# Kernel tuning notes

Hardware: AMD Instinct MI355X
Metric: run time of the kernel (lower is better)

Reference implementation:

```python
import jax, jax.numpy as jnp
import numpy as np

IMG = 32            # feature-map side == image_size
B, HC = 8, 3        # batch, hint channels
C, NH, L = 256, 8, 8  # model_channels, nhead, num_encoder_layers
DFF = 1025
HIN = IMG * 8       # hint resolution (three stride-2 convs => /8)
NEIGH = (7, 7)
CONV_SHAPES = [(16, HC), (16, 16), (32, 16), (32, 32), (96, 32), (96, 96), (256, 96), (C, 256)]
STRIDES = [1, 1, 2, 1, 2, 1, 2, 1]


def setup_inputs() -> dict:
    key = jax.random.key(0)
    ks = jax.random.split(key, 32)
    inp = {"hint": jax.random.normal(ks[0], (B, HC, HIN, HIN), jnp.float32)}
    for i, (co, ci) in enumerate(CONV_SHAPES):
        inp[f"conv_w{i}"] = jax.random.normal(ks[1 + i], (co, ci, 3, 3), jnp.float32) * 0.05
    base = 9
    def p(shape, j):
        return jax.random.normal(ks[base + j], (L,) + shape, jnp.float32) * 0.02
    inp["in_proj_w"] = p((3 * C, C), 0)
    inp["in_proj_b"] = p((3 * C,), 1)
    inp["out_w"] = p((C, C), 2)
    inp["out_b"] = p((C,), 3)
    inp["lin1_w"] = p((DFF, C), 4)
    inp["lin1_b"] = p((DFF,), 5)
    inp["lin2_w"] = p((C, DFF), 6)
    inp["lin2_b"] = p((C,), 7)
    inp["ln1_w"] = jnp.ones((L, C), jnp.float32)
    inp["ln1_b"] = jnp.zeros((L, C), jnp.float32)
    inp["ln2_w"] = jnp.ones((L, C), jnp.float32)
    inp["ln2_b"] = jnp.zeros((L, C), jnp.float32)
    return inp


def _conv(x, w, s):
    # torch Conv2d(k=3, padding=1, stride=s, bias=False)
    return jax.lax.conv_general_dilated(x, w, (s, s), [(1, 1), (1, 1)],
                                        dimension_numbers=("NCHW", "OIHW", "NCHW"))


def _sine_pos(h, w, c):
    # DETR/UniAD PositionEmbeddingSine (normalize=False, temperature=1e4) -> (h*w, c)
    npf = c // 2
    y = jnp.broadcast_to(jnp.arange(1, h + 1, dtype=jnp.float32)[:, None], (h, w))
    x = jnp.broadcast_to(jnp.arange(1, w + 1, dtype=jnp.float32)[None, :], (h, w))
    dim_t = 10000.0 ** (2.0 * (jnp.arange(npf, dtype=jnp.float32) // 2) / npf)
    px = x[..., None] / dim_t
    py = y[..., None] / dim_t
    px = jnp.stack([jnp.sin(px[..., 0::2]), jnp.cos(px[..., 1::2])], -1).reshape(h, w, npf)
    py = jnp.stack([jnp.sin(py[..., 0::2]), jnp.cos(py[..., 1::2])], -1).reshape(h, w, npf)
    return jnp.concatenate([py, px], -1).reshape(h * w, c)


def _neigh_mask(h, w, hm, wm):
    # vectorized version of generate_mask: 0 inside the hm x wm neighborhood, -inf outside
    ih = jnp.arange(h)
    iw = jnp.arange(w)
    dh = jnp.abs(ih[:, None] - ih[None, :]) <= hm // 2   # (h, h)
    dw = jnp.abs(iw[:, None] - iw[None, :]) <= wm // 2   # (w, w)
    allowed = (dh[:, None, :, None] & dw[None, :, None, :]).reshape(h * w, h * w)
    return jnp.where(allowed, 0.0, -1e9).astype(jnp.float32)


def _ln(x, g, b):
    mu = x.mean(-1, keepdims=True)
    v = ((x - mu) ** 2).mean(-1, keepdims=True)
    return (x - mu) / jnp.sqrt(v + 1e-5) * g + b


def _forward(hint, conv_ws, params):
    x = hint
    for i, (w, s) in enumerate(zip(conv_ws, STRIDES)):
        x = _conv(x, w, s)
        if i < len(conv_ws) - 1:
            x = jax.nn.silu(x)
    b, c, h, w = x.shape
    src = x.reshape(b, c, h * w).transpose(0, 2, 1)          # (B, N, C), N h-major
    pos = _sine_pos(h, w, c)[None]                           # (1, N, C)
    mask = _neigh_mask(h, w, *NEIGH)                         # (N, N)
    dh = c // NH
    scale = 1.0 / np.sqrt(dh).astype(np.float32)

    def layer(s, p):
        ipw, ipb, ow, ob, l1w, l1b, l2w, l2b, g1, b1, g2, b2 = p
        qk_in = s + pos
        q = (qk_in @ ipw[:c].T + ipb[:c]).reshape(b, -1, NH, dh)
        k = (qk_in @ ipw[c:2 * c].T + ipb[c:2 * c]).reshape(b, -1, NH, dh)
        v = (s @ ipw[2 * c:].T + ipb[2 * c:]).reshape(b, -1, NH, dh)
        sc = jnp.einsum('bnhd,bmhd->bhnm', q, k) * scale + mask
        a = jax.nn.softmax(sc, -1)
        ctx = jnp.einsum('bhnm,bmhd->bnhd', a, v).reshape(b, -1, c)
        s = _ln(s + ctx @ ow.T + ob, g1, b1)                 # post-norm
        ff = jax.nn.relu(s @ l1w.T + l1b) @ l2w.T + l2b      # dropout inactive (eval)
        return _ln(s + ff, g2, b2), None

    src, _ = jax.lax.scan(layer, src, params)
    return src.transpose(0, 2, 1).reshape(b, c, h, w)        # '(h w) b c -> b c h w'


def reference(hint, conv_w0, conv_w1, conv_w2, conv_w3, conv_w4, conv_w5, conv_w6, conv_w7,
              in_proj_w, in_proj_b, out_w, out_b, lin1_w, lin1_b, lin2_w, lin2_b,
              ln1_w, ln1_b, ln2_w, ln2_b):
    conv_ws = (conv_w0, conv_w1, conv_w2, conv_w3, conv_w4, conv_w5, conv_w6, conv_w7)
    params = (in_proj_w, in_proj_b, out_w, out_b, lin1_w, lin1_b, lin2_w, lin2_b,
              ln1_w, ln1_b, ln2_w, ln2_b)
    return _forward(hint, conv_ws, params)
```

## Files before the change

kernel.cpp:

```cpp
#include <hip/hip_runtime.h>
#include <hip/hip_bf16.h>


typedef __bf16 bf16x8 __attribute__((ext_vector_type(8)));
typedef float f32x4 __attribute__((ext_vector_type(4)));
typedef unsigned short us8v __attribute__((ext_vector_type(8)));

__device__ __forceinline__ unsigned short f2bf(float f) {
  unsigned int u = __float_as_uint(f);
  unsigned int r = (u + 0x7fffu + ((u >> 16) & 1u)) >> 16;
  return (unsigned short)r;
}
__device__ __forceinline__ float bf2f(unsigned short h) {
  return __uint_as_float(((unsigned int)h) << 16);
}

#define GLD16(src, dst)                                                        \
  __builtin_amdgcn_global_load_lds(                                            \
      (const __attribute__((address_space(1))) unsigned int*)(src),            \
      (__attribute__((address_space(3))) unsigned int*)(dst), 16, 0, 0)

template<int BM, int BN, int NT, int MODE, int LNF = 0, int KTC = 0>
__global__ __launch_bounds__(NT) void k_gemm(
    const unsigned short* __restrict__ A, int lda,
    const unsigned short* __restrict__ Bw, int ldb,
    const float* __restrict__ bias, const float* __restrict__ posadd,
    float* __restrict__ C, unsigned short* __restrict__ Cb, int ldc,
    int K, int Nstore, int act, int omode, long long zsB, long long zsC,
    const unsigned short* __restrict__ zpage, int Ci, int Hi, int stride, int lw,
    int divm, int divs, const float* __restrict__ lng, const float* __restrict__ lnb)
{
  constexpr int NW = NT / 64;
  constexpr int NWN = (NT == 512) ? 4 : ((BN >= 128) ? 2 : 1);
  constexpr int NWM = NW / NWN;
  constexpr int WM = BM / NWM, WN = BN / NWN;
  constexpr int MF = WM / 16, NF = WN / 16;
  constexpr int AIS = (BM * 8) / NT;
  constexpr int BIS = (BN * 8) / NT;
  __shared__ unsigned short lA[2][BM * 64];
  __shared__ unsigned short lB[2][BN * 64];
  __shared__ float red[2][32][2];
  int tid = threadIdx.x, lane = tid & 63, wid = tid >> 6;
  int bm = blockIdx.x * BM, bn = blockIdx.y * BN;
  const unsigned short* Bz = Bw + (size_t)blockIdx.z * zsB;

  int j = (lane & 7) ^ (lane >> 3);
  int e8 = (j & 3) << 3;
  int halfl = j >> 2;

  size_t arow[AIS], brow[BIS];
  int hb[AIS], wb[AIS];
  size_t ab[AIS];
#pragma unroll
  for (int i = 0; i < AIS; ++i) {
    int rr = (wid + i * NW) * 8 + (lane >> 3);
    if constexpr (MODE == 0) {
      arow[i] = (size_t)(bm + rr) * lda + (j << 3);
    } else {
      int pos = bm + rr;
      int b = pos >> (2 * lw);
      int rem = pos & ((1 << (2 * lw)) - 1);
      int ho = rem >> lw, wo = rem & ((1 << lw) - 1);
      hb[i] = ho * stride - 1;
      wb[i] = wo * stride - 1;
      ab[i] = (size_t)b * Hi * Hi * Ci;
    }
  }
#pragma unroll
  for (int i = 0; i < BIS; ++i)
    brow[i] = (size_t)(bn + (wid + i * NW) * 8 + (lane >> 3)) * ldb + (j << 3);

  auto stage = [&](int buf, int kt) {
    if constexpr (MODE == 1) {
      int s0 = kt * 2, s1 = s0 + 1;
      int t0 = (s0 * divm) >> divs, t1 = (s1 * divm) >> divs;
      int cipw = Ci >> 5;
      int cc0 = (s0 - t0 * cipw) << 5, cc1 = (s1 - t1 * cipw) << 5;
      int kh0 = (t0 * 171) >> 9, kw0 = t0 - kh0 * 3;
      int kh1 = (t1 * 171) >> 9, kw1 = t1 - kh1 * 3;
      int kh = halfl ? kh1 : kh0;
      int kw = halfl ? kw1 : kw0;
      int cco = halfl ? cc1 : cc0;
      bool tv = (halfl ? t1 : t0) < 9;
#pragma unroll
      for (int i = 0; i < AIS; ++i) {
        int hi = hb[i] + kh, wi = wb[i] + kw;
        const unsigned short* ap =
            (tv && (unsigned)hi < (unsigned)Hi && (unsigned)wi < (unsigned)Hi)
                ? (A + ab[i] + (size_t)(hi * Hi + wi) * Ci + cco + e8)
                : zpage;
        GLD16(ap, &lA[buf][(wid + i * NW) * 512]);
      }
    } else {
#pragma unroll
      for (int i = 0; i < AIS; ++i)
        GLD16(A + arow[i] + kt * 64, &lA[buf][(wid + i * NW) * 512]);
    }
#pragma unroll
    for (int i = 0; i < BIS; ++i)
      GLD16(Bz + brow[i] + kt * 64, &lB[buf][(wid + i * NW) * 512]);
  };

  f32x4 acc[MF][NF];
#pragma unroll
  for (int m = 0; m < MF; ++m)
#pragma unroll
    for (int n = 0; n < NF; ++n)
#pragma unroll
      for (int q = 0; q < 4; ++q) acc[m][n][q] = 0.f;

  int wn = wid % NWN, wm = wid / NWN;
  int r0 = wm * WM + (lane & 15);
  int c0 = wn * WN + (lane & 15);
  int sl0 = (((lane >> 4)) ^ (lane & 7)) << 3;
  int sl1 = (((lane >> 4) + 4) ^ (lane & 7)) << 3;
  const int nkt = (KTC > 0) ? KTC : (K >> 6);
  int cur = 0;
  stage(0, 0);
#pragma unroll
  for (int kt = 0; kt < nkt; ++kt) {
    if (kt + 1 < nkt) {
      stage(cur ^ 1, kt + 1);
      asm volatile("s_waitcnt vmcnt(%0)" : : "n"(AIS + BIS) : "memory");
    } else {
      asm volatile("s_waitcnt vmcnt(0)" : : : "memory");
    }
    __builtin_amdgcn_s_barrier();
    asm volatile("" ::: "memory");
    bf16x8 a0[MF], a1[MF], b0[NF], b1[NF];
#pragma unroll
    for (int m = 0; m < MF; ++m) {
      a0[m] = *(const bf16x8*)&lA[cur][(r0 + m * 16) * 64 + sl0];
      a1[m] = *(const bf16x8*)&lA[cur][(r0 + m * 16) * 64 + sl1];
    }
#pragma unroll
    for (int n = 0; n < NF; ++n) {
      b0[n] = *(const bf16x8*)&lB[cur][(c0 + n * 16) * 64 + sl0];
      b1[n] = *(const bf16x8*)&lB[cur][(c0 + n * 16) * 64 + sl1];
    }
#pragma unroll
    for (int m = 0; m < MF; ++m)
#pragma unroll
      for (int n = 0; n < NF; ++n)
        acc[m][n] = __builtin_amdgcn_mfma_f32_16x16x32_bf16(a0[m], b0[n], acc[m][n], 0, 0, 0);
#pragma unroll
    for (int m = 0; m < MF; ++m)
#pragma unroll
      for (int n = 0; n < NF; ++n)
        acc[m][n] = __builtin_amdgcn_mfma_f32_16x16x32_bf16(a1[m], b1[n], acc[m][n], 0, 0, 0);
    asm volatile("" ::: "memory");
    __builtin_amdgcn_s_barrier();
    cur ^= 1;
  }

  int colb = bn + wn * WN + (lane & 15);
  int rowb = bm + wm * WM + ((lane >> 4) << 2);

  if constexpr (LNF) {
    float x[NF][4];
    float sums[4] = {0.f, 0.f, 0.f, 0.f}, sqs[4] = {0.f, 0.f, 0.f, 0.f};
#pragma unroll
    for (int n = 0; n < NF; ++n) {
      int col = colb + n * 16;
      float bs = bias[col];
#pragma unroll
      for (int q = 0; q < 4; ++q) {
        int row = rowb + q;
        float v = acc[0][n][q] + bs + C[(size_t)row * 256 + col];
        x[n][q] = v;
        sums[q] += v;
        sqs[q] += v * v;
      }
    }
#pragma unroll
    for (int q = 0; q < 4; ++q) {
      sums[q] += __shfl_xor(sums[q], 1); sqs[q] += __shfl_xor(sqs[q], 1);
      sums[q] += __shfl_xor(sums[q], 2); sqs[q] += __shfl_xor(sqs[q], 2);
      sums[q] += __shfl_xor(sums[q], 4); sqs[q] += __shfl_xor(sqs[q], 4);
      sums[q] += __shfl_xor(sums[q], 8); sqs[q] += __shfl_xor(sqs[q], 8);
    }
    int rl = wm * 16 + ((lane >> 4) << 2);
    if ((lane & 15) == 0) {
#pragma unroll
      for (int q = 0; q < 4; ++q) {
        red[wn][rl + q][0] = sums[q];
        red[wn][rl + q][1] = sqs[q];
      }
    }
    __syncthreads();
#pragma unroll
    for (int q = 0; q < 4; ++q) {
      float ts = sums[q] + red[wn ^ 1][rl + q][0];
      float tq = sqs[q] + red[wn ^ 1][rl + q][1];
      float mu = ts * (1.f / 256.f);
      float var = tq * (1.f / 256.f) - mu * mu;
      float rs = rsqrtf(var + 1e-5f);
      int row = rowb + q;
#pragma unroll
      for (int n = 0; n < NF; ++n) {
        int col = colb + n * 16;
        float o = (x[n][q] - mu) * rs * lng[col] + lnb[col];
        C[(size_t)row * 256 + col] = o;
        Cb[(size_t)row * 256 + col] = f2bf(o);
      }
    }
    return;
  }

  float* Cz = C ? C + (size_t)blockIdx.z * zsC : nullptr;
  unsigned short* Cbz = Cb ? Cb + (size_t)blockIdx.z * zsC : nullptr;
#pragma unroll
  for (int n = 0; n < NF; ++n) {
    int col = colb + n * 16;
    if (col >= Nstore) continue;
    float bs = bias ? bias[col] : 0.f;
#pragma unroll
    for (int m = 0; m < MF; ++m) {
#pragma unroll
      for (int q = 0; q < 4; ++q) {
        int row = rowb + m * 16 + q;
        float v = acc[m][n][q] + bs;
        if (posadd && col < 512) v += posadd[((row & 1023) << 9) + col];
        if (act == 1) v = fmaxf(v, 0.f);
        else if (act == 2) v = v / (1.f + __expf(-v));
        size_t off = (size_t)row * ldc + col;
        if (omode == 0) Cz[off] = v;
        else if (omode == 1) Cbz[off] = f2bf(v);
        else { Cz[off] = v; Cbz[off] = f2bf(v); }
      }
    }
  }
}

__global__ __launch_bounds__(256) void k_ffn(
    const unsigned short* __restrict__ srcb, const unsigned short* __restrict__ w1,
    const float* __restrict__ b1, const unsigned short* __restrict__ w2,
    const float* __restrict__ b2, float* __restrict__ src,
    unsigned short* __restrict__ sbo,
    const float* __restrict__ lng, const float* __restrict__ lnb)
{
  __shared__ unsigned short aT[4][32 * 64];
  __shared__ unsigned short lB[2][256 * 64];
  __shared__ unsigned short ffl[32][1160];
  __shared__ float red[2][32][2];
  int tid = threadIdx.x, lane = tid & 63, wid = tid >> 6;
  int bm = blockIdx.x << 5;
  int j = (lane & 7) ^ (lane >> 3);
  int rsrc = (lane >> 3);

  {
    int rr = wid * 8 + rsrc;
    const unsigned short* ap = srcb + (size_t)(bm + rr) * 256 + (j << 3);
#pragma unroll
    for (int kt = 0; kt < 4; ++kt)
      GLD16(ap + kt * 64, &aT[kt][wid * 512]);
  }
  size_t brow1[4], brow2[8];
#pragma unroll
  for (int i = 0; i < 4; ++i)
    brow1[i] = (size_t)((wid + i * 4) * 8 + rsrc) * 256 + (j << 3);
#pragma unroll
  for (int i = 0; i < 8; ++i)
    brow2[i] = (size_t)((wid + i * 4) * 8 + rsrc) * 1152 + (j << 3);

  auto stageB1 = [&](int buf, int s) {
    int ny = s >> 2, kt = s & 3;
#pragma unroll
    for (int i = 0; i < 4; ++i)
      GLD16(w1 + (size_t)ny * 128 * 256 + brow1[i] + kt * 64, &lB[buf][(wid + i * 4) * 512]);
  };
  auto stageB2 = [&](int buf, int kt) {
#pragma unroll
    for (int i = 0; i < 8; ++i)
      GLD16(w2 + brow2[i] + kt * 64, &lB[buf][(wid + i * 4) * 512]);
  };

  int wn = wid & 1, wm = wid >> 1;
  int r0 = wm * 16 + (lane & 15);
  int sl0 = (((lane >> 4)) ^ (lane & 7)) << 3;
  int sl1 = (((lane >> 4) + 4) ^ (lane & 7)) << 3;
  int kqa = (lane >> 4) << 3;

  stageB1(0, 0);
  int cur = 0;
  for (int ny = 0; ny < 9; ++ny) {
    f32x4 acc1[4];
#pragma unroll
    for (int n = 0; n < 4; ++n)
#pragma unroll
      for (int q = 0; q < 4; ++q) acc1[n][q] = 0.f;
    int c01 = wn * 64 + (lane & 15);
#pragma unroll
    for (int kt = 0; kt < 4; ++kt) {
      int s = ny * 4 + kt;
      if (s + 1 < 36) {
        stageB1(cur ^ 1, s + 1);
        asm volatile("s_waitcnt vmcnt(4)" : : : "memory");
      } else {
        asm volatile("s_waitcnt vmcnt(0)" : : : "memory");
      }
      __builtin_amdgcn_s_barrier();
      asm volatile("" ::: "memory");
      bf16x8 a0 = *(const bf16x8*)&aT[kt][r0 * 64 + sl0];
      bf16x8 a1 = *(const bf16x8*)&aT[kt][r0 * 64 + sl1];
      bf16x8 b0v[4], b1v[4];
#pragma unroll
      for (int n = 0; n < 4; ++n) {
        b0v[n] = *(const bf16x8*)&lB[cur][(c01 + n * 16) * 64 + sl0];
        b1v[n] = *(const bf16x8*)&lB[cur][(c01 + n * 16) * 64 + sl1];
      }
#pragma unroll
      for (int n = 0; n < 4; ++n)
        acc1[n] = __builtin_amdgcn_mfma_f32_16x16x32_bf16(a0, b0v[n], acc1[n], 0, 0, 0);
#pragma unroll
      for (int n = 0; n < 4; ++n)
        acc1[n] = __builtin_amdgcn_mfma_f32_16x16x32_bf16(a1, b1v[n], acc1[n], 0, 0, 0);
      asm volatile("" ::: "memory");
      __builtin_amdgcn_s_barrier();
      cur ^= 1;
    }
    int rowl = wm * 16 + ((lane >> 4) << 2);
#pragma unroll
    for (int n = 0; n < 4; ++n) {
      int col = ny * 128 + c01 + n * 16;
      float bs = b1[col];
#pragma unroll
      for (int q = 0; q < 4; ++q)
        ffl[rowl + q][col] = f2bf(fmaxf(acc1[n][q] + bs, 0.f));
    }
  }

  stageB2(0, 0);
  __syncthreads();
  cur = 0;
  f32x4 acc[8];
#pragma unroll
  for (int n = 0; n < 8; ++n)
#pragma unroll
    for (int q = 0; q < 4; ++q) acc[n][q] = 0.f;
  int c02 = wn * 128 + (lane & 15);
#pragma unroll
  for (int kt = 0; kt < 18; ++kt) {
    if (kt + 1 < 18) {
      stageB2(cur ^ 1, kt + 1);
      asm volatile("s_waitcnt vmcnt(8)" : : : "memory");
    } else {
      asm volatile("s_waitcnt vmcnt(0)" : : : "memory");
    }
    __builtin_amdgcn_s_barrier();
    asm volatile("" ::: "memory");
    bf16x8 a0 = *(const bf16x8*)&ffl[r0][kt * 64 + kqa];
    bf16x8 a1 = *(const bf16x8*)&ffl[r0][kt * 64 + 32 + kqa];
    bf16x8 b0v[8], b1v[8];
#pragma unroll
    for (int n = 0; n < 8; ++n) {
      b0v[n] = *(const bf16x8*)&lB[cur][(c02 + n * 16) * 64 + sl0];
      b1v[n] = *(const bf16x8*)&lB[cur][(c02 + n * 16) * 64 + sl1];
    }
#pragma unroll
    for (int n = 0; n < 8; ++n)
      acc[n] = __builtin_amdgcn_mfma_f32_16x16x32_bf16(a0, b0v[n], acc[n], 0, 0, 0);
#pragma unroll
    for (int n = 0; n < 8; ++n)
      acc[n] = __builtin_amdgcn_mfma_f32_16x16x32_bf16(a1, b1v[n], acc[n], 0, 0, 0);
    asm volatile("" ::: "memory");
    __builtin_amdgcn_s_barrier();
    cur ^= 1;
  }

  int rowl = wm * 16 + ((lane >> 4) << 2);
  float x[8][4];
  float sums[4] = {0.f, 0.f, 0.f, 0.f}, sqs[4] = {0.f, 0.f, 0.f, 0.f};
#pragma unroll
  for (int n = 0; n < 8; ++n) {
    int col = c02 + n * 16;
    float bs = b2[col];
#pragma unroll
    for (int q = 0; q < 4; ++q) {
      int row = bm + rowl + q;
      float v = acc[n][q] + bs + src[(size_t)row * 256 + col];
      x[n][q] = v;
      sums[q] += v;
      sqs[q] += v * v;
    }
  }
#pragma unroll
  for (int q = 0; q < 4; ++q) {
    sums[q] += __shfl_xor(sums[q], 1); sqs[q] += __shfl_xor(sqs[q], 1);
    sums[q] += __shfl_xor(sums[q], 2); sqs[q] += __shfl_xor(sqs[q], 2);
    sums[q] += __shfl_xor(sums[q], 4); sqs[q] += __shfl_xor(sqs[q], 4);
    sums[q] += __shfl_xor(sums[q], 8); sqs[q] += __shfl_xor(sqs[q], 8);
  }
  if ((lane & 15) == 0) {
#pragma unroll
    for (int q = 0; q < 4; ++q) {
      red[wn][rowl + q][0] = sums[q];
      red[wn][rowl + q][1] = sqs[q];
    }
  }
  __syncthreads();
#pragma unroll
  for (int q = 0; q < 4; ++q) {
    float ts = sums[q] + red[wn ^ 1][rowl + q][0];
    float tq = sqs[q] + red[wn ^ 1][rowl + q][1];
    float mu = ts * (1.f / 256.f);
    float var = tq * (1.f / 256.f) - mu * mu;
    float rs = rsqrtf(var + 1e-5f);
    int row = bm + rowl + q;
#pragma unroll
    for (int n = 0; n < 8; ++n) {
      int col = c02 + n * 16;
      float o = (x[n][q] - mu) * rs * lng[col] + lnb[col];
      src[(size_t)row * 256 + col] = o;
      sbo[(size_t)row * 256 + col] = f2bf(o);
    }
  }
}

__global__ __launch_bounds__(256) void k_conv0(
    const float* __restrict__ x, const float* __restrict__ w,
    unsigned short* __restrict__ y)
{
  __shared__ float ws[16][28];
  int tid = threadIdx.x;
  for (int u = tid; u < 432; u += 256) {
    int co = u / 27, k = u - co * 27;
    int t = k / 3, ci = k - t * 3;
    ws[co][k] = w[((size_t)co * 3 + ci) * 9 + t];
  }
  __syncthreads();
  int h = blockIdx.x, b = blockIdx.y, wo = tid;
  float xin[3][3][3];
#pragma unroll
  for (int ci = 0; ci < 3; ++ci)
#pragma unroll
    for (int kh = 0; kh < 3; ++kh) {
      int hi = h + kh - 1;
#pragma unroll
      for (int kw = 0; kw < 3; ++kw) {
        int wi = wo + kw - 1;
        xin[ci][kh][kw] = ((unsigned)hi < 256u && (unsigned)wi < 256u)
            ? x[(((size_t)b * 3 + ci) << 16) + (hi << 8) + wi] : 0.f;
      }
    }
  float acc[16] = {};
#pragma unroll
  for (int t = 0; t < 9; ++t) {
    const int kh = t / 3, kw = t % 3;
#pragma unroll
    for (int ci = 0; ci < 3; ++ci) {
      float xv = xin[ci][kh][kw];
#pragma unroll
      for (int co = 0; co < 16; ++co)
        acc[co] = fmaf(xv, ws[co][t * 3 + ci], acc[co]);
    }
  }
  us8v o0, o1, zv;
#pragma unroll
  for (int q = 0; q < 8; ++q) {
    float v0 = acc[q];     v0 = v0 / (1.f + __expf(-v0)); o0[q] = f2bf(v0);
    float v1 = acc[q + 8]; v1 = v1 / (1.f + __expf(-v1)); o1[q] = f2bf(v1);
    zv[q] = 0;
  }
  unsigned short* yp = y + ((((size_t)b << 16) + (h << 8) + wo) << 5);
  *(us8v*)(yp) = o0; *(us8v*)(yp + 8) = o1;
  *(us8v*)(yp + 16) = zv; *(us8v*)(yp + 24) = zv;
}

template<int S>
__global__ __launch_bounds__(256) void k_conv_direct(
    const unsigned short* __restrict__ x, const unsigned short* __restrict__ wp,
    int ldw, unsigned short* __restrict__ y, int Hi, int Ho, int Wo, int lwt)
{
  constexpr int HR = 7 * S + 3;
  constexpr int HC = 15 * S + 3;
  constexpr int HP = HR * HC;
  __shared__ unsigned short xs[HP * 40];
  __shared__ unsigned short wsh[32 * 312];
  int tid = threadIdx.x, lane = tid & 63, wv = tid >> 6;
  int b = blockIdx.y;
  int tr = blockIdx.x >> lwt, tc = blockIdx.x & ((1 << lwt) - 1);
  int hi0 = tr * 8 * S - 1, wi0 = tc * 16 * S - 1;

  for (int u = tid; u < HP * 8; u += 256) {
    int pix = u >> 3, part = u & 7;
    int hr = pix / HC, hcc = pix - hr * HC;
    int hi = hi0 + hr, wi = wi0 + hcc;
    ushort4 v = {0, 0, 0, 0};
    if ((unsigned)hi < (unsigned)Hi && (unsigned)wi < (unsigned)Hi)
      v = *(const ushort4*)(x + ((size_t)(b * Hi + hi) * Hi + wi) * 32 + part * 4);
    *(ushort4*)(&xs[pix * 40 + part * 4]) = v;
  }
  for (int u = tid; u < 2304; u += 256) {
    int co = u / 72, kk = (u - co * 72) * 4;
    *(ushort4*)(&wsh[co * 312 + kk]) = *(const ushort4*)(wp + (size_t)co * ldw + kk);
  }
  __syncthreads();

  int cL = lane & 15, kq = (lane >> 4) << 3;
  f32x4 acc[2][2];
#pragma unroll
  for (int m = 0; m < 2; ++m)
#pragma unroll
    for (int n = 0; n < 2; ++n)
#pragma unroll
      for (int q = 0; q < 4; ++q) acc[m][n][q] = 0.f;

#pragma unroll
  for (int tap = 0; tap < 9; ++tap) {
    const int kh = tap / 3, kw = tap % 3;
    bf16x8 af[2], bfr[2];
#pragma unroll
    for (int m = 0; m < 2; ++m) {
      int hr = (wv * 2 + m) * S + kh;
      int hc = cL * S + kw;
      af[m] = *(const bf16x8*)&xs[(hr * HC + hc) * 40 + kq];
    }
#pragma unroll
    for (int n = 0; n < 2; ++n)
      bfr[n] = *(const bf16x8*)&wsh[(cL + n * 16) * 312 + tap * 32 + kq];
#pragma unroll
    for (int m = 0; m < 2; ++m)
#pragma unroll
      for (int n = 0; n < 2; ++n)
        acc[m][n] = __builtin_amdgcn_mfma_f32_16x16x32_bf16(af[m], bfr[n], acc[m][n], 0, 0, 0);
  }

  int wo0 = tc * 16 + ((lane >> 4) << 2);
#pragma unroll
  for (int m = 0; m < 2; ++m) {
    int ho = tr * 8 + wv * 2 + m;
#pragma unroll
    for (int n = 0; n < 2; ++n) {
      int co = cL + n * 16;
#pragma unroll
      for (int q = 0; q < 4; ++q) {
        float v = acc[m][n][q];
        v = v / (1.f + __expf(-v));
        y[((size_t)(b * Ho + ho) * Wo + wo0 + q) * 32 + co] = f2bf(v);
      }
    }
  }
}

struct WP8 { const float* w[8]; unsigned short* q[8]; };
__global__ __launch_bounds__(256) void k_wperm_all(WP8 p)
{
  const int CoPs[8]  = {128, 32, 32, 32, 128, 128, 256, 256};
  const int CiRs[8]  = {3, 16, 16, 32, 32, 96, 96, 256};
  const int CiPs[8]  = {3, 32, 32, 32, 32, 96, 96, 256};
  const int Kpads[8] = {64, 288, 288, 288, 320, 896, 896, 2304};
  const int Cos[8]   = {16, 16, 32, 32, 96, 96, 256, 256};
  int i = blockIdx.y + 1;
  const float* w = p.w[i];
  unsigned short* wp = p.q[i];
  int Kpad = Kpads[i], CiP = CiPs[i], CiR = CiRs[i], Co = Cos[i];
  int total = CoPs[i] * Kpad;
  for (int idx = blockIdx.x * 256 + threadIdx.x; idx < total; idx += gridDim.x * 256) {
    int co = idx / Kpad, k = idx - co * Kpad;
    int t = k / CiP, ci = k - t * CiP;
    float v = 0.f;
    if (co < Co && t < 9 && ci < CiR) v = w[((size_t)co * CiR + ci) * 9 + t];
    wp[idx] = f2bf(v);
  }
}

struct PrepArgs {
  const float *ipw, *outw, *l1w, *l2w, *l1b;
  unsigned short *wqkvb, *outwb, *l1wb, *l2wb, *posb;
  float *l1bp;
};
__global__ __launch_bounds__(256) void k_prep(PrepArgs a)
{
  int seg = blockIdx.y;
  int idx0 = blockIdx.x * 256 + threadIdx.x;
  int stride = gridDim.x * 256;
  if (seg == 0) {
    for (int i = idx0; i < 8 * 768 * 256; i += stride) a.wqkvb[i] = f2bf(a.ipw[i]);
  } else if (seg == 1) {
    for (int i = idx0; i < 8 * 256 * 256; i += stride) a.outwb[i] = f2bf(a.outw[i]);
  } else if (seg == 2) {
    for (int i = idx0; i < 8 * 1152 * 256; i += stride) {
      int l = i / (1152 * 256), r = (i >> 8) % 1152, c = i & 255;
      float v = (r < 1025) ? a.l1w[((size_t)l * 1025 + r) * 256 + c] : 0.f;
      a.l1wb[i] = f2bf(v);
    }
  } else if (seg == 3) {
    for (int i = idx0; i < 8 * 256 * 1152; i += stride) {
      int l = i / (256 * 1152), rc = i % (256 * 1152), r = rc / 1152, c = rc - (rc / 1152) * 1152;
      float v = (c < 1025) ? a.l2w[((size_t)l * 256 + r) * 1025 + c] : 0.f;
      a.l2wb[i] = f2bf(v);
    }
  } else if (seg == 4) {
    for (int i = idx0; i < 8 * 1152; i += stride) {
      int l = i / 1152, c = i - l * 1152;
      a.l1bp[i] = (c < 1025) ? a.l1b[l * 1025 + c] : 0.f;
    }
  } else {
    for (int i = idx0; i < 1024 * 256; i += stride) {
      int n = i >> 8, c = i & 255;
      int ih = n >> 5, iw = n & 31;
      float coord = (c < 128) ? (float)(ih + 1) : (float)(iw + 1);
      int cc = c & 127;
      float e = (float)((cc >> 1) << 1) * (1.f / 128.f);
      float t = coord / powf(10000.f, e);
      a.posb[i] = f2bf((cc & 1) ? cosf(t) : sinf(t));
    }
  }
}

__global__ __launch_bounds__(256) void k_attn(
    const unsigned short* __restrict__ qkv, unsigned short* __restrict__ ctx)
{
  __shared__ unsigned short k_ldsu[848 * 8];
  __shared__ unsigned short v_lds[848 * 8];
  __shared__ float p_lds[64 * 50];
  int bx = blockIdx.x;
  int b = bx >> 4, tile = bx & 15;
  int th8 = ((tile >> 2) << 3), tw8 = ((tile & 3) << 3);
  int g = blockIdx.y;
  int tid = threadIdx.x, lane = tid & 63, wid = tid >> 6;
  int h0e = max(th8 - 3, 0), h1e = min(th8 + 10, 31);
  int w0e = max(tw8 - 3, 0), w1e = min(tw8 + 10, 31);
  int nh = h1e - h0e + 1, nw = w1e - w0e + 1;
  int nkeys = nh * nw, nslots = nkeys * 4;
  unsigned int magic = (65536u + (unsigned)nw - 1u) / (unsigned)nw;
  size_t qbase = (size_t)((unsigned)b << 10) * 768;

#pragma unroll
  for (int i = 0; i < 4; ++i) {
    int base = i * 256 + wid * 64;
    if (base < 784) {
      int s = min(base + lane, nslots - 1);
      int uidx = s >> 2, chunk = s & 3;
      int hh = (int)(((unsigned)uidx * magic) >> 16);
      int ww = uidx - hh * nw;
      hh += h0e; ww += w0e;
      const unsigned short* rp = qkv + qbase + (size_t)((hh << 5) + ww) * 768 + (g << 5) + chunk * 8;
      GLD16(rp + 256, &k_ldsu[base * 8]);
      GLD16(rp + 512, &v_lds[base * 8]);
    }
  }
  __syncthreads();

  int q = tid >> 2, dq = tid & 3;
  int qh = th8 + (q >> 3), qw = tw8 + (q & 7);
  const float scale = 0.17677669529663687f;
  const unsigned short* qp = qkv + qbase + (size_t)((qh << 5) + qw) * 768 + (g << 5) + dq * 8;
  us8v uq = *(const us8v*)qp;
  float qr[8];
#pragma unroll
  for (int t = 0; t < 8; ++t) qr[t] = bf2f(uq[t]) * scale;

  int rbase[7], cofs[7];
  bool rval[7], cval[7];
#pragma unroll
  for (int d = 0; d < 7; ++d) {
    int mh = qh - 3 + d;
    rval[d] = (unsigned)mh < 32u;
    rbase[d] = (mh - h0e) * nw;
    int mw = qw - 3 + d;
    cval[d] = (unsigned)mw < 32u;
    cofs[d] = mw - w0e;
  }

  float m = -1e30f;
#pragma unroll
  for (int kk = 0; kk < 49; ++kk) {
    const int d7 = kk / 7, r7 = kk % 7;
    bool valid = rval[d7] && cval[r7];
    int uidx = valid ? (rbase[d7] + cofs[r7]) : 0;
    us8v uk = *(const us8v*)&k_ldsu[uidx * 32 + dq * 8];
    float d = 0.f;
#pragma unroll
    for (int t = 0; t < 8; ++t) d = fmaf(qr[t], bf2f(uk[t]), d);
    d += __shfl_xor(d, 1);
    d += __shfl_xor(d, 2);
    float s_kk = valid ? d : -1e30f;
    m = fmaxf(m, s_kk);
    if (dq == (kk & 3)) p_lds[q * 50 + kk] = s_kk;
  }
  float sum = 0.f;
  for (int kk = dq; kk < 49; kk += 4) {
    float e = __expf(p_lds[q * 50 + kk] - m);
    p_lds[q * 50 + kk] = e;
    sum += e;
  }
  sum += __shfl_xor(sum, 1);
  sum += __shfl_xor(sum, 2);
  float inv = 1.f / sum;

  float acc[8] = {};
#pragma unroll
  for (int kk = 0; kk < 49; ++kk) {
    const int d7 = kk / 7, r7 = kk % 7;
    int uidx = (rval[d7] && cval[r7]) ? (rbase[d7] + cofs[r7]) : 0;
    float pb = p_lds[q * 50 + kk];
    us8v uv = *(const us8v*)&v_lds[uidx * 32 + dq * 8];
#pragma unroll
    for (int t = 0; t < 8; ++t) acc[t] = fmaf(pb, bf2f(uv[t]), acc[t]);
  }
  unsigned short* op = ctx + ((size_t)((b << 10) + (qh << 5) + qw) << 8) + (g << 5) + dq * 8;
  us8v out;
#pragma unroll
  for (int t = 0; t < 8; ++t) out[t] = f2bf(acc[t] * inv);
  *(us8v*)op = out;
}

__global__ void k_nxc_to_cxn(const float* __restrict__ x, float* __restrict__ y)
{
  __shared__ float t[32][33];
  int b = blockIdx.z;
  int c0 = blockIdx.x * 32, n0 = blockIdx.y * 32;
  int tx = threadIdx.x, ty = threadIdx.y;
  t[ty][tx] = x[((size_t)(b * 1024 + n0 + ty)) * 256 + c0 + tx];
  __syncthreads();
  y[((size_t)(b * 256 + c0 + ty)) * 1024 + n0 + tx] = t[tx][ty];
}

extern "C" void kernel_launch(void* const* d_in, const int* in_sizes, int n_in,
                              void* d_out, int out_size, void* d_ws, size_t ws_size,
                              hipStream_t stream)
{
  const float* hint = (const float*)d_in[0];
  const float* cw[8];
  for (int i = 0; i < 8; ++i) cw[i] = (const float*)d_in[1 + i];
  const float* ipw  = (const float*)d_in[9];
  const float* ipb  = (const float*)d_in[10];
  const float* outw = (const float*)d_in[11];
  const float* outb = (const float*)d_in[12];
  const float* l1w  = (const float*)d_in[13];
  const float* l1b  = (const float*)d_in[14];
  const float* l2w  = (const float*)d_in[15];
  const float* l2b  = (const float*)d_in[16];
  const float* g1   = (const float*)d_in[17];
  const float* b1   = (const float*)d_in[18];
  const float* g2   = (const float*)d_in[19];
  const float* b2   = (const float*)d_in[20];

  float* ws = (float*)d_ws;
  size_t off = 0;
  float* bufA = ws + off; off += 8388608;
  float* bufB = ws + off; off += 8388608;
  float* src  = ws + off; off += 2097152;
  unsigned short* srcb = (unsigned short*)(ws + off); off += 1048576;
  unsigned short* posb = (unsigned short*)(ws + off); off += 131072;
  float* posqk = ws + off; off += 4194304;
  unsigned short* wqkvb = (unsigned short*)(ws + off); off += 786432;
  unsigned short* outwb = (unsigned short*)(ws + off); off += 262144;
  unsigned short* l1wb  = (unsigned short*)(ws + off); off += 1179648;
  unsigned short* l2wb  = (unsigned short*)(ws + off); off += 1179648;
  float* l1bp = ws + off; off += 9216;
  unsigned short* cwp[8];
  const int CoPs[8]  = {128, 32, 32, 32, 128, 128, 256, 256};
  const int Kpads[8] = {64, 288, 288, 288, 320, 896, 896, 2304};
  for (int i = 0; i < 8; ++i) { cwp[i] = (unsigned short*)(ws + off); off += ((size_t)CoPs[i] * Kpads[i] + 1) / 2; }
  unsigned short* zpage = (unsigned short*)(ws + off); off += 64;

  hipMemsetAsync(zpage, 0, 256, stream);

  PrepArgs pa;
  pa.ipw = ipw; pa.outw = outw; pa.l1w = l1w; pa.l2w = l2w; pa.l1b = l1b;
  pa.wqkvb = wqkvb; pa.outwb = outwb; pa.l1wb = l1wb; pa.l2wb = l2wb;
  pa.posb = posb; pa.l1bp = l1bp;
  k_prep<<<dim3(256, 6), 256, 0, stream>>>(pa);
  WP8 wpargs;
  for (int i = 0; i < 8; ++i) { wpargs.w[i] = cw[i]; wpargs.q[i] = cwp[i]; }
  k_wperm_all<<<dim3(64, 7), 256, 0, stream>>>(wpargs);

  unsigned short* bufAu = (unsigned short*)bufA;
  unsigned short* bufBu = (unsigned short*)bufB;

#define GEMM_TAIL nullptr, 0, 0, 0, 0, 0, 0, nullptr, nullptr
  k_conv0<<<dim3(256, 8), 256, 0, stream>>>(hint, cw[0], bufAu);
  k_conv_direct<1><<<dim3(512, 8), 256, 0, stream>>>(bufAu, cwp[1], 288, bufBu, 256, 256, 256, 4);
  k_conv_direct<2><<<dim3(128, 8), 256, 0, stream>>>(bufBu, cwp[2], 288, bufAu, 256, 128, 128, 3);
  k_conv_direct<1><<<dim3(128, 8), 256, 0, stream>>>(bufAu, cwp[3], 288, bufBu, 128, 128, 128, 3);
  k_gemm<128, 128, 512, 1, 0, 5><<<dim3(256, 1), 512, 0, stream>>>(
      bufBu, 0, cwp[4], 320, nullptr, nullptr, nullptr, bufAu, 96, 320, 96, 2, 1,
      0, 0, zpage, 32, 128, 2, 6, 1, 0, nullptr, nullptr);
  k_gemm<128, 128, 512, 1, 0, 14><<<dim3(256, 1), 512, 0, stream>>>(
      bufAu, 0, cwp[5], 896, nullptr, nullptr, nullptr, bufBu, 96, 896, 96, 2, 1,
      0, 0, zpage, 96, 64, 1, 6, 171, 9, nullptr, nullptr);
  k_gemm<64, 128, 512, 1, 0, 14><<<dim3(128, 2), 512, 0, stream>>>(
      bufBu, 0, cwp[6], 896, nullptr, nullptr, nullptr, bufAu, 256, 896, 256, 2, 1,
      0, 0, zpage, 96, 64, 2, 5, 171, 9, nullptr, nullptr);
  k_gemm<64, 128, 512, 1><<<dim3(128, 2), 512, 0, stream>>>(
      bufAu, 0, cwp[7], 2304, nullptr, nullptr, src, srcb, 256, 2304, 256, 0, 2,
      0, 0, zpage, 256, 32, 1, 5, 1, 3, nullptr, nullptr);

  k_gemm<64, 128, 512, 0, 0, 4><<<dim3(16, 4, 8), 512, 0, stream>>>(
      posb, 256, wqkvb, 256, nullptr, nullptr, posqk, nullptr, 512, 256, 512, 0, 0,
      196608LL, 524288LL, GEMM_TAIL);

  unsigned short* qkvb = bufAu;
  unsigned short* ctx  = (unsigned short*)(bufA + 3145728);

  for (int l = 0; l < 8; ++l) {
    const unsigned short* wqkv_l = wqkvb + (size_t)l * 768 * 256;
    const float* ipb_l  = ipb  + (size_t)l * 768;
    const unsigned short* outw_l = outwb + (size_t)l * 256 * 256;
    const float* outb_l = outb + (size_t)l * 256;
    const unsigned short* l1w_l = l1wb + (size_t)l * 1152 * 256;
    const float* l1b_l  = l1bp + (size_t)l * 1152;
    const unsigned short* l2w_l = l2wb + (size_t)l * 256 * 1152;
    const float* l2b_l  = l2b  + (size_t)l * 256;
    const float* posqk_l = posqk + (size_t)l * 524288;
    const float* g1_l = g1 + l * 256; const float* b1_l = b1 + l * 256;
    const float* g2_l = g2 + l * 256; const float* b2_l = b2 + l * 256;

    k_gemm<64, 128, 512, 0, 0, 4><<<dim3(128, 6), 512, 0, stream>>>(
        srcb, 256, wqkv_l, 256, ipb_l, posqk_l, nullptr, qkvb, 768, 256, 768, 0, 1,
        0, 0, GEMM_TAIL);
    k_attn<<<dim3(128, 8), 256, 0, stream>>>(qkvb, ctx);
    k_gemm<32, 256, 256, 0, 1, 4><<<dim3(256, 1), 256, 0, stream>>>(
        ctx, 256, outw_l, 256, outb_l, nullptr, src, srcb, 256, 256, 256, 0, 0,
        0, 0, nullptr, 0, 0, 0, 0, 0, 0, g1_l, b1_l);
    k_ffn<<<dim3(256), 256, 0, stream>>>(
        srcb, l1w_l, l1b_l, l2w_l, l2b_l, src, srcb, g2_l, b2_l);
  }

  k_nxc_to_cxn<<<dim3(8, 32, 8), dim3(32, 32), 0, stream>>>(src, (float*)d_out);
}
```

Baseline: 887.0 us.

## Fuse out-projection and first LayerNorm into the FFN kernel

Replaces the separate out-projection GEMM with LayerNorm epilogue and the FFN kernel with a single kernel per 32-row block. The block computes ctx@Wo, adds bias and residual, applies LN1, writes the normalized bf16 rows back into its shared A tile, keeps the fp32 residual in registers and then runs the FFN and LN2. This removes one launch per layer and the global round trip of src/srcb between the two stages. The cost is higher register pressure from the extra residual array, and the Wo weights are now streamed by every block inside the fused kernel.

```diff
diff --git a/kernel.cpp b/kernel.cpp
--- a/kernel.cpp
+++ b/kernel.cpp
@@ -39,7 +39,6 @@
   constexpr int BIS = (BN * 8) / NT;
   __shared__ unsigned short lA[2][BM * 64];
   __shared__ unsigned short lB[2][BN * 64];
-  __shared__ float red[2][32][2];
   int tid = threadIdx.x, lane = tid & 63, wid = tid >> 6;
   int bm = blockIdx.x * BM, bn = blockIdx.y * BN;
   const unsigned short* Bz = Bw + (size_t)blockIdx.z * zsB;
@@ -155,58 +154,6 @@
 
   int colb = bn + wn * WN + (lane & 15);
   int rowb = bm + wm * WM + ((lane >> 4) << 2);
-
-  if constexpr (LNF) {
-    float x[NF][4];
-    float sums[4] = {0.f, 0.f, 0.f, 0.f}, sqs[4] = {0.f, 0.f, 0.f, 0.f};
-#pragma unroll
-    for (int n = 0; n < NF; ++n) {
-      int col = colb + n * 16;
-      float bs = bias[col];
-#pragma unroll
-      for (int q = 0; q < 4; ++q) {
-        int row = rowb + q;
-        float v = acc[0][n][q] + bs + C[(size_t)row * 256 + col];
-        x[n][q] = v;
-        sums[q] += v;
-        sqs[q] += v * v;
-      }
-    }
-#pragma unroll
-    for (int q = 0; q < 4; ++q) {
-      sums[q] += __shfl_xor(sums[q], 1); sqs[q] += __shfl_xor(sqs[q], 1);
-      sums[q] += __shfl_xor(sums[q], 2); sqs[q] += __shfl_xor(sqs[q], 2);
-      sums[q] += __shfl_xor(sums[q], 4); sqs[q] += __shfl_xor(sqs[q], 4);
-      sums[q] += __shfl_xor(sums[q], 8); sqs[q] += __shfl_xor(sqs[q], 8);
-    }
-    int rl = wm * 16 + ((lane >> 4) << 2);
-    if ((lane & 15) == 0) {
-#pragma unroll
-      for (int q = 0; q < 4; ++q) {
-        red[wn][rl + q][0] = sums[q];
-        red[wn][rl + q][1] = sqs[q];
-      }
-    }
-    __syncthreads();
-#pragma unroll
-    for (int q = 0; q < 4; ++q) {
-      float ts = sums[q] + red[wn ^ 1][rl + q][0];
-      float tq = sqs[q] + red[wn ^ 1][rl + q][1];
-      float mu = ts * (1.f / 256.f);
-      float var = tq * (1.f / 256.f) - mu * mu;
-      float rs = rsqrtf(var + 1e-5f);
-      int row = rowb + q;
-#pragma unroll
-      for (int n = 0; n < NF; ++n) {
-        int col = colb + n * 16;
-        float o = (x[n][q] - mu) * rs * lng[col] + lnb[col];
-        C[(size_t)row * 256 + col] = o;
-        Cb[(size_t)row * 256 + col] = f2bf(o);
-      }
-    }
-    return;
-  }
-
   float* Cz = C ? C + (size_t)blockIdx.z * zsC : nullptr;
   unsigned short* Cbz = Cb ? Cb + (size_t)blockIdx.z * zsC : nullptr;
 #pragma unroll
@@ -232,12 +179,14 @@
   }
 }
 
-__global__ __launch_bounds__(256) void k_ffn(
-    const unsigned short* __restrict__ srcb, const unsigned short* __restrict__ w1,
-    const float* __restrict__ b1, const unsigned short* __restrict__ w2,
-    const float* __restrict__ b2, float* __restrict__ src,
-    unsigned short* __restrict__ sbo,
-    const float* __restrict__ lng, const float* __restrict__ lnb)
+__global__ __launch_bounds__(256) void k_mlp(
+    const unsigned short* __restrict__ ctx, const unsigned short* __restrict__ wo,
+    const float* __restrict__ ob,
+    const unsigned short* __restrict__ w1, const float* __restrict__ b1,
+    const unsigned short* __restrict__ w2, const float* __restrict__ b2,
+    float* __restrict__ src, unsigned short* __restrict__ sbo,
+    const float* __restrict__ g1, const float* __restrict__ lb1,
+    const float* __restrict__ g2, const float* __restrict__ lb2)
 {
   __shared__ unsigned short aT[4][32 * 64];
   __shared__ unsigned short lB[2][256 * 64];
@@ -246,43 +195,136 @@
   int tid = threadIdx.x, lane = tid & 63, wid = tid >> 6;
   int bm = blockIdx.x << 5;
   int j = (lane & 7) ^ (lane >> 3);
-  int rsrc = (lane >> 3);
+  int rsrc = lane >> 3;
 
   {
     int rr = wid * 8 + rsrc;
-    const unsigned short* ap = srcb + (size_t)(bm + rr) * 256 + (j << 3);
+    const unsigned short* ap = ctx + (size_t)(bm + rr) * 256 + (j << 3);
 #pragma unroll
     for (int kt = 0; kt < 4; ++kt)
       GLD16(ap + kt * 64, &aT[kt][wid * 512]);
   }
-  size_t brow1[4], brow2[8];
-#pragma unroll
-  for (int i = 0; i < 4; ++i)
-    brow1[i] = (size_t)((wid + i * 4) * 8 + rsrc) * 256 + (j << 3);
-#pragma unroll
-  for (int i = 0; i < 8; ++i)
-    brow2[i] = (size_t)((wid + i * 4) * 8 + rsrc) * 1152 + (j << 3);
-
+  size_t brow256[8], brow1152[8];
+#pragma unroll
+  for (int i = 0; i < 8; ++i) {
+    int rr = (wid + i * 4) * 8 + rsrc;
+    brow256[i]  = (size_t)rr * 256 + (j << 3);
+    brow1152[i] = (size_t)rr * 1152 + (j << 3);
+  }
+  auto stageWo = [&](int buf, int kt) {
+#pragma unroll
+    for (int i = 0; i < 8; ++i)
+      GLD16(wo + brow256[i] + kt * 64, &lB[buf][(wid + i * 4) * 512]);
+  };
   auto stageB1 = [&](int buf, int s) {
     int ny = s >> 2, kt = s & 3;
 #pragma unroll
     for (int i = 0; i < 4; ++i)
-      GLD16(w1 + (size_t)ny * 128 * 256 + brow1[i] + kt * 64, &lB[buf][(wid + i * 4) * 512]);
+      GLD16(w1 + (size_t)ny * 128 * 256 + brow256[i] + kt * 64, &lB[buf][(wid + i * 4) * 512]);
   };
   auto stageB2 = [&](int buf, int kt) {
 #pragma unroll
     for (int i = 0; i < 8; ++i)
-      GLD16(w2 + brow2[i] + kt * 64, &lB[buf][(wid + i * 4) * 512]);
+      GLD16(w2 + brow1152[i] + kt * 64, &lB[buf][(wid + i * 4) * 512]);
   };
 
   int wn = wid & 1, wm = wid >> 1;
   int r0 = wm * 16 + (lane & 15);
-  int sl0 = (((lane >> 4)) ^ (lane & 7)) << 3;
+  int sl0 = ((lane >> 4) ^ (lane & 7)) << 3;
   int sl1 = (((lane >> 4) + 4) ^ (lane & 7)) << 3;
   int kqa = (lane >> 4) << 3;
-
+  int c02 = wn * 128 + (lane & 15);
+  int rowl = wm * 16 + ((lane >> 4) << 2);
+
+  stageWo(0, 0);
+  int cur = 0;
+  f32x4 acco[8];
+#pragma unroll
+  for (int n = 0; n < 8; ++n)
+#pragma unroll
+    for (int q = 0; q < 4; ++q) acco[n][q] = 0.f;
+#pragma unroll
+  for (int kt = 0; kt < 4; ++kt) {
+    if (kt + 1 < 4) {
+      stageWo(cur ^ 1, kt + 1);
+      asm volatile("s_waitcnt vmcnt(8)" : : : "memory");
+    } else {
+      asm volatile("s_waitcnt vmcnt(0)" : : : "memory");
+    }
+    __builtin_amdgcn_s_barrier();
+    asm volatile("" ::: "memory");
+    bf16x8 a0 = *(const bf16x8*)&aT[kt][r0 * 64 + sl0];
+    bf16x8 a1 = *(const bf16x8*)&aT[kt][r0 * 64 + sl1];
+    bf16x8 b0v[8], b1v[8];
+#pragma unroll
+    for (int n = 0; n < 8; ++n) {
+      b0v[n] = *(const bf16x8*)&lB[cur][(c02 + n * 16) * 64 + sl0];
+      b1v[n] = *(const bf16x8*)&lB[cur][(c02 + n * 16) * 64 + sl1];
+    }
+#pragma unroll
+    for (int n = 0; n < 8; ++n)
+      acco[n] = __builtin_amdgcn_mfma_f32_16x16x32_bf16(a0, b0v[n], acco[n], 0, 0, 0);
+#pragma unroll
+    for (int n = 0; n < 8; ++n)
+      acco[n] = __builtin_amdgcn_mfma_f32_16x16x32_bf16(a1, b1v[n], acco[n], 0, 0, 0);
+    asm volatile("" ::: "memory");
+    __builtin_amdgcn_s_barrier();
+    cur ^= 1;
+  }
   stageB1(0, 0);
-  int cur = 0;
+
+  float resid[8][4];
+  {
+    float x[8][4];
+    float sums[4] = {0.f, 0.f, 0.f, 0.f}, sqs[4] = {0.f, 0.f, 0.f, 0.f};
+#pragma unroll
+    for (int n = 0; n < 8; ++n) {
+      int col = c02 + n * 16;
+      float bs = ob[col];
+#pragma unroll
+      for (int q = 0; q < 4; ++q) {
+        float v = acco[n][q] + bs + src[(size_t)(bm + rowl + q) * 256 + col];
+        x[n][q] = v;
+        sums[q] += v;
+        sqs[q] += v * v;
+      }
+    }
+#pragma unroll
+    for (int q = 0; q < 4; ++q) {
+      sums[q] += __shfl_xor(sums[q], 1); sqs[q] += __shfl_xor(sqs[q], 1);
+      sums[q] += __shfl_xor(sums[q], 2); sqs[q] += __shfl_xor(sqs[q], 2);
+      sums[q] += __shfl_xor(sums[q], 4); sqs[q] += __shfl_xor(sqs[q], 4);
+      sums[q] += __shfl_xor(sums[q], 8); sqs[q] += __shfl_xor(sqs[q], 8);
+    }
+    if ((lane & 15) == 0) {
+#pragma unroll
+      for (int q = 0; q < 4; ++q) {
+        red[wn][rowl + q][0] = sums[q];
+        red[wn][rowl + q][1] = sqs[q];
+      }
+    }
+    __syncthreads();
+#pragma unroll
+    for (int q = 0; q < 4; ++q) {
+      float ts = sums[q] + red[wn ^ 1][rowl + q][0];
+      float tq = sqs[q] + red[wn ^ 1][rowl + q][1];
+      float mu = ts * (1.f / 256.f);
+      float var = tq * (1.f / 256.f) - mu * mu;
+      float rs = rsqrtf(var + 1e-5f);
+      int r = rowl + q;
+#pragma unroll
+      for (int n = 0; n < 8; ++n) {
+        int col = c02 + n * 16;
+        float o = (x[n][q] - mu) * rs * g1[col] + lb1[col];
+        resid[n][q] = o;
+        int kt = col >> 6, jj = (col >> 3) & 7, e = col & 7;
+        aT[kt][r * 64 + (((jj ^ (r & 7))) << 3) + e] = f2bf(o);
+      }
+    }
+  }
+  __syncthreads();
+
+  cur = 0;
   for (int ny = 0; ny < 9; ++ny) {
     f32x4 acc1[4];
 #pragma unroll
@@ -319,14 +361,14 @@
       __builtin_amdgcn_s_barrier();
       cur ^= 1;
     }
-    int rowl = wm * 16 + ((lane >> 4) << 2);
+    int rowe = wm * 16 + ((lane >> 4) << 2);
 #pragma unroll
     for (int n = 0; n < 4; ++n) {
       int col = ny * 128 + c01 + n * 16;
       float bs = b1[col];
 #pragma unroll
       for (int q = 0; q < 4; ++q)
-        ffl[rowl + q][col] = f2bf(fmaxf(acc1[n][q] + bs, 0.f));
+        ffl[rowe + q][col] = f2bf(fmaxf(acc1[n][q] + bs, 0.f));
     }
   }
 
@@ -338,7 +380,6 @@
   for (int n = 0; n < 8; ++n)
 #pragma unroll
     for (int q = 0; q < 4; ++q) acc[n][q] = 0.f;
-  int c02 = wn * 128 + (lane & 15);
 #pragma unroll
   for (int kt = 0; kt < 18; ++kt) {
     if (kt + 1 < 18) {
@@ -368,7 +409,6 @@
     cur ^= 1;
   }
 
-  int rowl = wm * 16 + ((lane >> 4) << 2);
   float x[8][4];
   float sums[4] = {0.f, 0.f, 0.f, 0.f}, sqs[4] = {0.f, 0.f, 0.f, 0.f};
 #pragma unroll
@@ -377,8 +417,7 @@
     float bs = b2[col];
 #pragma unroll
     for (int q = 0; q < 4; ++q) {
-      int row = bm + rowl + q;
-      float v = acc[n][q] + bs + src[(size_t)row * 256 + col];
+      float v = acc[n][q] + bs + resid[n][q];
       x[n][q] = v;
       sums[q] += v;
       sqs[q] += v * v;
@@ -410,7 +449,7 @@
 #pragma unroll
     for (int n = 0; n < 8; ++n) {
       int col = c02 + n * 16;
-      float o = (x[n][q] - mu) * rs * lng[col] + lnb[col];
+      float o = (x[n][q] - mu) * rs * g2[col] + lb2[col];
       src[(size_t)row * 256 + col] = o;
       sbo[(size_t)row * 256 + col] = f2bf(o);
     }
@@ -813,11 +852,9 @@
         srcb, 256, wqkv_l, 256, ipb_l, posqk_l, nullptr, qkvb, 768, 256, 768, 0, 1,
         0, 0, GEMM_TAIL);
     k_attn<<<dim3(128, 8), 256, 0, stream>>>(qkvb, ctx);
-    k_gemm<32, 256, 256, 0, 1, 4><<<dim3(256, 1), 256, 0, stream>>>(
-        ctx, 256, outw_l, 256, outb_l, nullptr, src, srcb, 256, 256, 256, 0, 0,
-        0, 0, nullptr, 0, 0, 0, 0, 0, 0, g1_l, b1_l);
-    k_ffn<<<dim3(256), 256, 0, stream>>>(
-        srcb, l1w_l, l1b_l, l2w_l, l2b_l, src, srcb, g2_l, b2_l);
+    k_mlp<<<dim3(256), 256, 0, stream>>>(
+        ctx, outw_l, outb_l, l1w_l, l1b_l, l2w_l, l2b_l,
+        src, srcb, g1_l, b1_l, g2_l, b2_l);
   }
 
   k_nxc_to_cxn<<<dim3(8, 32, 8), dim3(32, 32), 0, stream>>>(src, (float*)d_out);
```

Result: faster. 849.8 us (-4.2%).
